# Optimization experiments

Measured on AMD Instinct MI355X. Metric: run time of the kernel, lower is better.

## Reference

```python
import jax, jax.numpy as jnp
import numpy as np

EPS = 1e-8
HALF_BIN = 0.1 / 2.0  # discretization_param / 2


def setup_inputs() -> dict:
    key = jax.random.key(0)
    k1, k2, k3, k4, k5, k6 = jax.random.split(key, 6)
    B, K = 4194304, 3
    predicted_purchase_prob = jax.random.uniform(k1, (B,), jnp.float32, 0.01, 0.99)
    mu = jax.random.normal(k2, (K, B), jnp.float32) * 5.0 + 10.0
    sigma = jax.random.uniform(k3, (K, B), jnp.float32, 0.1, 2.0)
    weight = jax.random.uniform(k4, (K, B), jnp.float32, 0.0, 1.0)
    paid = jax.random.uniform(k5, (B,)) > 0.5
    vals = jax.random.uniform(k6, (B,), jnp.float32, 0.1, 50.0)
    true_values = jnp.where(paid, vals, 0.0)
    return {
        "predicted_purchase_prob": predicted_purchase_prob,
        "mu": mu,
        "sigma": sigma,
        "weight": weight,
        "true_values": true_values,
    }


def reference(predicted_purchase_prob, mu, sigma, weight, true_values):
    p = predicted_purchase_prob  # [B]
    targets = (true_values > 0).astype(p.dtype)  # [B]
    # BCE with torch-style log clamping at -100
    log_p = jnp.clip(jnp.log(p + 0.0), -100.0)
    log_1mp = jnp.clip(jnp.log(1.0 - p), -100.0)
    purchase_loss = -jnp.mean(targets * log_p + (1.0 - targets) * log_1mp)

    # Mixture-of-logistics discretized likelihood, vectorized over [K, B]
    inv_s = 1.0 / (sigma + EPS)  # [K, B]
    tv = true_values[None, :]  # [1, B]
    cdf_upper = jax.nn.sigmoid((tv + HALF_BIN - mu) * inv_s)
    cdf_lower = jax.nn.sigmoid((tv - HALF_BIN - mu) * inv_s)
    prob_density = jnp.maximum(cdf_upper - cdf_lower, EPS)  # clamp(min=1e-8)
    likelihood = jnp.sum(weight * prob_density, axis=0)  # [B]
    log_likelihood = jnp.log(likelihood + EPS)  # [B]

    paid_mask = true_values > 0
    n_paid = jnp.sum(paid_mask.astype(p.dtype))
    ll_sum = jnp.sum(jnp.where(paid_mask, log_likelihood, 0.0))
    ltv_loss = -jnp.where(n_paid > 0, ll_sum / jnp.maximum(n_paid, 1.0), 0.0)

    return purchase_loss + ltv_loss
```

## Files before the change

### kernel.cpp

```cpp
#include <hip/hip_runtime.h>
#include <math.h>

#define EPS 1e-8f
#define HALF_BIN 0.05f

typedef float v4f __attribute__((ext_vector_type(4)));

#define GLOAD4(dst, addr) \
    asm("global_load_dwordx4 %0, %1, off" : "=v"(dst) : "v"(addr))

__device__ __forceinline__ float sigmoid_diff(float xu, float xl) {
    float eu = __expf(fminf(-xu, 87.0f));
    float el = __expf(fminf(-xl, 87.0f));
    return __fdividef(el - eu, (1.0f + eu) * (1.0f + el));
}

__device__ __forceinline__ void accum4(
    const v4f& pf, const v4f& tf,
    const v4f& m0, const v4f& s0, const v4f& w0,
    const v4f& m1, const v4f& s1, const v4f& w1,
    const v4f& m2, const v4f& s2, const v4f& w2,
    float& bce, float& ll, float& npaid)
{
    float lik[4] = {0.0f, 0.0f, 0.0f, 0.0f};
    const v4f* mm[3] = {&m0, &m1, &m2};
    const v4f* ss[3] = {&s0, &s1, &s2};
    const v4f* ww[3] = {&w0, &w1, &w2};
    #pragma unroll
    for (int k = 0; k < 3; ++k) {
        const v4f m = *mm[k], s = *ss[k], w = *ww[k];
        #pragma unroll
        for (int j = 0; j < 4; ++j) {
            float inv_s = __fdividef(1.0f, s[j] + EPS);
            float xu = (tf[j] + HALF_BIN - m[j]) * inv_s;
            float xl = (tf[j] - HALF_BIN - m[j]) * inv_s;
            float pd = fmaxf(sigmoid_diff(xu, xl), EPS);
            lik[j] = fmaf(w[j], pd, lik[j]);
        }
    }
    #pragma unroll
    for (int j = 0; j < 4; ++j) {
        bool paid = tf[j] > 0.0f;
        float val = paid ? pf[j] : (1.0f - pf[j]);
        bce -= fmaxf(__logf(val), -100.0f);
        float lg = __logf(lik[j] + EPS);
        ll    += paid ? lg : 0.0f;
        npaid += paid ? 1.0f : 0.0f;
    }
}

__global__ __launch_bounds__(256, 4) void zimol_main_k3(
    const float* __restrict__ p,
    const float* __restrict__ mu,
    const float* __restrict__ sigma,
    const float* __restrict__ weight,
    const float* __restrict__ tv,
    float* __restrict__ part_bce,
    float* __restrict__ part_ll,
    float* __restrict__ part_n,
    int B)
{
    const int tid    = blockIdx.x * blockDim.x + threadIdx.x;
    const int stride = gridDim.x * blockDim.x;
    const size_t B4  = (size_t)(B >> 2);

    const v4f* __restrict__ p4  = (const v4f*)p;
    const v4f* __restrict__ tv4 = (const v4f*)tv;
    const v4f* __restrict__ mu4 = (const v4f*)mu;
    const v4f* __restrict__ sg4 = (const v4f*)sigma;
    const v4f* __restrict__ wt4 = (const v4f*)weight;

    float bce = 0.0f, ll = 0.0f, npaid = 0.0f;

    for (size_t i = (size_t)tid; i < B4; i += (size_t)stride) {
        v4f bp, bt, bm0, bs0, bw0, bm1, bs1, bw1, bm2, bs2, bw2;
        GLOAD4(bp,  p4  + i);
        GLOAD4(bt,  tv4 + i);
        GLOAD4(bm0, mu4 + i);
        GLOAD4(bs0, sg4 + i);
        GLOAD4(bw0, wt4 + i);
        GLOAD4(bm1, mu4 + B4 + i);
        GLOAD4(bs1, sg4 + B4 + i);
        GLOAD4(bw1, wt4 + B4 + i);
        GLOAD4(bm2, mu4 + 2 * B4 + i);
        GLOAD4(bs2, sg4 + 2 * B4 + i);
        GLOAD4(bw2, wt4 + 2 * B4 + i);
        asm volatile("s_waitcnt vmcnt(0)"
                     : "+v"(bp), "+v"(bt),
                       "+v"(bm0), "+v"(bs0), "+v"(bw0),
                       "+v"(bm1), "+v"(bs1), "+v"(bw1),
                       "+v"(bm2), "+v"(bs2), "+v"(bw2));
        accum4(bp, bt, bm0, bs0, bw0, bm1, bs1, bw1, bm2, bs2, bw2,
               bce, ll, npaid);
    }

    #pragma unroll
    for (int off = 32; off > 0; off >>= 1) {
        bce   += __shfl_down(bce,   off, 64);
        ll    += __shfl_down(ll,    off, 64);
        npaid += __shfl_down(npaid, off, 64);
    }
    __shared__ float sdata[3][4];
    const int wave = threadIdx.x >> 6;
    const int lane = threadIdx.x & 63;
    if (lane == 0) {
        sdata[0][wave] = bce; sdata[1][wave] = ll; sdata[2][wave] = npaid;
    }
    __syncthreads();
    if (threadIdx.x == 0) {
        float b = 0.0f, l = 0.0f, n = 0.0f;
        #pragma unroll
        for (int w = 0; w < 4; ++w) {
            b += sdata[0][w]; l += sdata[1][w]; n += sdata[2][w];
        }
        part_bce[blockIdx.x] = b;
        part_ll [blockIdx.x] = l;
        part_n  [blockIdx.x] = n;
    }
}

template <int K>
__global__ __launch_bounds__(256) void zimol_main_gen(
    const float* __restrict__ p,
    const float* __restrict__ mu,
    const float* __restrict__ sigma,
    const float* __restrict__ weight,
    const float* __restrict__ tv,
    float* __restrict__ part_bce,
    float* __restrict__ part_ll,
    float* __restrict__ part_n,
    int B)
{
    const int tid    = blockIdx.x * blockDim.x + threadIdx.x;
    const int stride = gridDim.x * blockDim.x;

    float bce = 0.0f, ll = 0.0f, npaid = 0.0f;

    for (int i = tid; i < B; i += stride) {
        float t = tv[i];
        float lik = 0.0f;
        #pragma unroll
        for (int k = 0; k < K; ++k) {
            size_t off = (size_t)k * (size_t)B + (size_t)i;
            float inv_s = __fdividef(1.0f, sigma[off] + EPS);
            float xu = (t + HALF_BIN - mu[off]) * inv_s;
            float xl = (t - HALF_BIN - mu[off]) * inv_s;
            float pd = fmaxf(sigmoid_diff(xu, xl), EPS);
            lik = fmaf(weight[off], pd, lik);
        }
        bool paid = t > 0.0f;
        float val = paid ? p[i] : (1.0f - p[i]);
        bce -= fmaxf(__logf(val), -100.0f);
        float lg = __logf(lik + EPS);
        ll    += paid ? lg : 0.0f;
        npaid += paid ? 1.0f : 0.0f;
    }

    #pragma unroll
    for (int off = 32; off > 0; off >>= 1) {
        bce   += __shfl_down(bce,   off, 64);
        ll    += __shfl_down(ll,    off, 64);
        npaid += __shfl_down(npaid, off, 64);
    }
    __shared__ float sdata[3][4];
    const int wave = threadIdx.x >> 6;
    const int lane = threadIdx.x & 63;
    if (lane == 0) {
        sdata[0][wave] = bce; sdata[1][wave] = ll; sdata[2][wave] = npaid;
    }
    __syncthreads();
    if (threadIdx.x == 0) {
        float b = 0.0f, l = 0.0f, n = 0.0f;
        #pragma unroll
        for (int w = 0; w < 4; ++w) {
            b += sdata[0][w]; l += sdata[1][w]; n += sdata[2][w];
        }
        part_bce[blockIdx.x] = b;
        part_ll [blockIdx.x] = l;
        part_n  [blockIdx.x] = n;
    }
}

__global__ __launch_bounds__(256) void zimol_reduce(
    const float* __restrict__ part_bce,
    const float* __restrict__ part_ll,
    const float* __restrict__ part_n,
    float* __restrict__ out, int nblocks, int B)
{
    double b = 0.0, l = 0.0, n = 0.0;
    for (int i = threadIdx.x; i < nblocks; i += 256) {
        b += (double)part_bce[i];
        l += (double)part_ll[i];
        n += (double)part_n[i];
    }
    #pragma unroll
    for (int off = 32; off > 0; off >>= 1) {
        b += __shfl_down(b, off, 64);
        l += __shfl_down(l, off, 64);
        n += __shfl_down(n, off, 64);
    }
    __shared__ double sdata[3][4];
    const int wave = threadIdx.x >> 6;
    const int lane = threadIdx.x & 63;
    if (lane == 0) {
        sdata[0][wave] = b; sdata[1][wave] = l; sdata[2][wave] = n;
    }
    __syncthreads();
    if (threadIdx.x == 0) {
        double tb = 0.0, tl = 0.0, tn = 0.0;
        #pragma unroll
        for (int w = 0; w < 4; ++w) {
            tb += sdata[0][w]; tl += sdata[1][w]; tn += sdata[2][w];
        }
        double purchase = tb / (double)B;
        double ltv = (tn > 0.0) ? -(tl / fmax(tn, 1.0)) : 0.0;
        out[0] = (float)(purchase + ltv);
    }
}

extern "C" void kernel_launch(void* const* d_in, const int* in_sizes, int n_in,
                              void* d_out, int out_size, void* d_ws, size_t ws_size,
                              hipStream_t stream) {
    const float* p      = (const float*)d_in[0];
    const float* mu     = (const float*)d_in[1];
    const float* sigma  = (const float*)d_in[2];
    const float* weight = (const float*)d_in[3];
    const float* tv     = (const float*)d_in[4];
    float* out = (float*)d_out;

    const int B = in_sizes[0];
    const int K = in_sizes[1] / B;

    const int threads = 256;
    int blocks;

    float* part_bce = (float*)d_ws;

    if (K == 3 && (B & 3) == 0) {
        int work = B >> 2;
        blocks = (work + threads - 1) / threads;
        if (blocks > 2048) blocks = 2048;
        if (blocks < 1) blocks = 1;
        float* part_ll = part_bce + blocks;
        float* part_n  = part_ll  + blocks;
        zimol_main_k3<<<blocks, threads, 0, stream>>>(
            p, mu, sigma, weight, tv, part_bce, part_ll, part_n, B);
        zimol_reduce<<<1, threads, 0, stream>>>(part_bce, part_ll, part_n, out, blocks, B);
    } else {
        blocks = (B + threads - 1) / threads;
        if (blocks > 2048) blocks = 2048;
        if (blocks < 1) blocks = 1;
        float* part_ll = part_bce + blocks;
        float* part_n  = part_ll  + blocks;
        if (K == 1) {
            zimol_main_gen<1><<<blocks, threads, 0, stream>>>(
                p, mu, sigma, weight, tv, part_bce, part_ll, part_n, B);
        } else if (K == 2) {
            zimol_main_gen<2><<<blocks, threads, 0, stream>>>(
                p, mu, sigma, weight, tv, part_bce, part_ll, part_n, B);
        } else if (K == 3) {
            zimol_main_gen<3><<<blocks, threads, 0, stream>>>(
                p, mu, sigma, weight, tv, part_bce, part_ll, part_n, B);
        } else {
            zimol_main_gen<4><<<blocks, threads, 0, stream>>>(
                p, mu, sigma, weight, tv, part_bce, part_ll, part_n, B);
        }
        zimol_reduce<<<1, threads, 0, stream>>>(part_bce, part_ll, part_n, out, blocks, B);
    }
}
```

Measured before the change: 198.3 us.

## Double-buffer tiles in LDS via global_load_lds with wave-split async loads

Replaces direct per-thread dwordx4 register loads with asynchronous global-to-LDS loads (global_load_lds) into a double-buffered 512-element tile, split across the four waves. The next tile is prefetched while the current one is computed, using vmcnt waits and barriers for ordering. The grid is fixed at 768 blocks. This is meant to overlap memory latency with the transcendental-heavy compute, at the cost of two barriers per tile and a larger LDS footprint, which may lower occupancy.

```diff
diff --git a/kernel.cpp b/kernel.cpp
--- a/kernel.cpp
+++ b/kernel.cpp
@@ -4,10 +4,11 @@
 #define EPS 1e-8f
 #define HALF_BIN 0.05f
 
-typedef float v4f __attribute__((ext_vector_type(4)));
-
-#define GLOAD4(dst, addr) \
-    asm("global_load_dwordx4 %0, %1, off" : "=v"(dst) : "v"(addr))
+#define TILE 512
+#define BUF_FLOATS (11 * TILE)
+#define SMEM_FLOATS (2 * BUF_FLOATS)
+
+typedef float v2f __attribute__((ext_vector_type(2)));
 
 __device__ __forceinline__ float sigmoid_diff(float xu, float xl) {
     float eu = __expf(fminf(-xu, 87.0f));
@@ -15,41 +16,51 @@
     return __fdividef(el - eu, (1.0f + eu) * (1.0f + el));
 }
 
-__device__ __forceinline__ void accum4(
-    const v4f& pf, const v4f& tf,
-    const v4f& m0, const v4f& s0, const v4f& w0,
-    const v4f& m1, const v4f& s1, const v4f& w1,
-    const v4f& m2, const v4f& s2, const v4f& w2,
-    float& bce, float& ll, float& npaid)
+__device__ __forceinline__ void ld_unit(const float* gsrc, float* ldst_uniform) {
+    __builtin_amdgcn_global_load_lds(
+        (const __attribute__((address_space(1))) void*)gsrc,
+        (__attribute__((address_space(3))) void*)ldst_uniform,
+        16, 0, 0);
+}
+
+__device__ __forceinline__ void issue_tile(
+    const float* p, const float* tv,
+    const float* mu0, const float* sg0, const float* wt0,
+    const float* mu1, const float* sg1, const float* wt1,
+    const float* mu2, const float* sg2, const float* wt2,
+    float* lb, int tstart, int wave, int lane)
 {
-    float lik[4] = {0.0f, 0.0f, 0.0f, 0.0f};
-    const v4f* mm[3] = {&m0, &m1, &m2};
-    const v4f* ss[3] = {&s0, &s1, &s2};
-    const v4f* ww[3] = {&w0, &w1, &w2};
-    #pragma unroll
-    for (int k = 0; k < 3; ++k) {
-        const v4f m = *mm[k], s = *ss[k], w = *ww[k];
-        #pragma unroll
-        for (int j = 0; j < 4; ++j) {
-            float inv_s = __fdividef(1.0f, s[j] + EPS);
-            float xu = (tf[j] + HALF_BIN - m[j]) * inv_s;
-            float xl = (tf[j] - HALF_BIN - m[j]) * inv_s;
-            float pd = fmaxf(sigmoid_diff(xu, xl), EPS);
-            lik[j] = fmaf(w[j], pd, lik[j]);
-        }
-    }
-    #pragma unroll
-    for (int j = 0; j < 4; ++j) {
-        bool paid = tf[j] > 0.0f;
-        float val = paid ? pf[j] : (1.0f - pf[j]);
-        bce -= fmaxf(__logf(val), -100.0f);
-        float lg = __logf(lik[j] + EPS);
-        ll    += paid ? lg : 0.0f;
-        npaid += paid ? 1.0f : 0.0f;
-    }
-}
-
-__global__ __launch_bounds__(256, 4) void zimol_main_k3(
+    const int l4 = lane * 4;
+    if (wave == 0) {
+        ld_unit(p   + tstart       + l4, lb + 0);
+        ld_unit(p   + tstart + 256 + l4, lb + 256);
+        ld_unit(tv  + tstart       + l4, lb + 512);
+        ld_unit(tv  + tstart + 256 + l4, lb + 768);
+        ld_unit(mu0 + tstart       + l4, lb + 1024);
+        ld_unit(mu0 + tstart + 256 + l4, lb + 1280);
+    } else if (wave == 1) {
+        ld_unit(sg0 + tstart       + l4, lb + 1536);
+        ld_unit(sg0 + tstart + 256 + l4, lb + 1792);
+        ld_unit(wt0 + tstart       + l4, lb + 2048);
+        ld_unit(wt0 + tstart + 256 + l4, lb + 2304);
+        ld_unit(mu1 + tstart       + l4, lb + 2560);
+        ld_unit(mu1 + tstart + 256 + l4, lb + 2816);
+    } else if (wave == 2) {
+        ld_unit(sg1 + tstart       + l4, lb + 3072);
+        ld_unit(sg1 + tstart + 256 + l4, lb + 3328);
+        ld_unit(wt1 + tstart       + l4, lb + 3584);
+        ld_unit(wt1 + tstart + 256 + l4, lb + 3840);
+        ld_unit(mu2 + tstart       + l4, lb + 4096);
+    } else {
+        ld_unit(mu2 + tstart + 256 + l4, lb + 4352);
+        ld_unit(sg2 + tstart       + l4, lb + 4608);
+        ld_unit(sg2 + tstart + 256 + l4, lb + 4864);
+        ld_unit(wt2 + tstart       + l4, lb + 5120);
+        ld_unit(wt2 + tstart + 256 + l4, lb + 5376);
+    }
+}
+
+__global__ __launch_bounds__(256) void zimol_main_k3(
     const float* __restrict__ p,
     const float* __restrict__ mu,
     const float* __restrict__ sigma,
@@ -60,38 +71,84 @@
     float* __restrict__ part_n,
     int B)
 {
-    const int tid    = blockIdx.x * blockDim.x + threadIdx.x;
-    const int stride = gridDim.x * blockDim.x;
-    const size_t B4  = (size_t)(B >> 2);
-
-    const v4f* __restrict__ p4  = (const v4f*)p;
-    const v4f* __restrict__ tv4 = (const v4f*)tv;
-    const v4f* __restrict__ mu4 = (const v4f*)mu;
-    const v4f* __restrict__ sg4 = (const v4f*)sigma;
-    const v4f* __restrict__ wt4 = (const v4f*)weight;
+    __shared__ float smem[SMEM_FLOATS];
+
+    const int wave = threadIdx.x >> 6;
+    const int lane = threadIdx.x & 63;
+    const int nt   = B / TILE;
+    const int G    = gridDim.x;
+
+    const float* mu0 = mu;
+    const float* mu1 = mu + (size_t)B;
+    const float* mu2 = mu + 2 * (size_t)B;
+    const float* sg0 = sigma;
+    const float* sg1 = sigma + (size_t)B;
+    const float* sg2 = sigma + 2 * (size_t)B;
+    const float* wt0 = weight;
+    const float* wt1 = weight + (size_t)B;
+    const float* wt2 = weight + 2 * (size_t)B;
 
     float bce = 0.0f, ll = 0.0f, npaid = 0.0f;
 
-    for (size_t i = (size_t)tid; i < B4; i += (size_t)stride) {
-        v4f bp, bt, bm0, bs0, bw0, bm1, bs1, bw1, bm2, bs2, bw2;
-        GLOAD4(bp,  p4  + i);
-        GLOAD4(bt,  tv4 + i);
-        GLOAD4(bm0, mu4 + i);
-        GLOAD4(bs0, sg4 + i);
-        GLOAD4(bw0, wt4 + i);
-        GLOAD4(bm1, mu4 + B4 + i);
-        GLOAD4(bs1, sg4 + B4 + i);
-        GLOAD4(bw1, wt4 + B4 + i);
-        GLOAD4(bm2, mu4 + 2 * B4 + i);
-        GLOAD4(bs2, sg4 + 2 * B4 + i);
-        GLOAD4(bw2, wt4 + 2 * B4 + i);
-        asm volatile("s_waitcnt vmcnt(0)"
-                     : "+v"(bp), "+v"(bt),
-                       "+v"(bm0), "+v"(bs0), "+v"(bw0),
-                       "+v"(bm1), "+v"(bs1), "+v"(bw1),
-                       "+v"(bm2), "+v"(bs2), "+v"(bw2));
-        accum4(bp, bt, bm0, bs0, bw0, bm1, bs1, bw1, bm2, bs2, bw2,
-               bce, ll, npaid);
+    int t   = blockIdx.x;
+    int buf = 0;
+    if (t < nt)
+        issue_tile(p, tv, mu0, sg0, wt0, mu1, sg1, wt1, mu2, sg2, wt2,
+                   smem, t * TILE, wave, lane);
+
+    for (; t < nt; t += G) {
+        const int tn = t + G;
+        if (tn < nt) {
+            issue_tile(p, tv, mu0, sg0, wt0, mu1, sg1, wt1, mu2, sg2, wt2,
+                       smem + (buf ^ 1) * BUF_FLOATS, tn * TILE, wave, lane);
+            if (wave < 2) asm volatile("s_waitcnt vmcnt(6)" ::: "memory");
+            else          asm volatile("s_waitcnt vmcnt(5)" ::: "memory");
+        } else {
+            asm volatile("s_waitcnt vmcnt(0)" ::: "memory");
+        }
+        asm volatile("s_barrier" ::: "memory");
+
+        const float* lb = smem + buf * BUF_FLOATS;
+        const int e = 2 * threadIdx.x;
+
+        v2f P = *(const v2f*)(lb + 0   + e);
+        v2f T = *(const v2f*)(lb + 512 + e);
+        v2f M[3], S[3], W[3];
+        M[0] = *(const v2f*)(lb + 1024 + e);
+        S[0] = *(const v2f*)(lb + 1536 + e);
+        W[0] = *(const v2f*)(lb + 2048 + e);
+        M[1] = *(const v2f*)(lb + 2560 + e);
+        S[1] = *(const v2f*)(lb + 3072 + e);
+        W[1] = *(const v2f*)(lb + 3584 + e);
+        M[2] = *(const v2f*)(lb + 4096 + e);
+        S[2] = *(const v2f*)(lb + 4608 + e);
+        W[2] = *(const v2f*)(lb + 5120 + e);
+
+        float lik[2] = {0.0f, 0.0f};
+        #pragma unroll
+        for (int k = 0; k < 3; ++k) {
+            #pragma unroll
+            for (int j = 0; j < 2; ++j) {
+                float inv_s = __fdividef(1.0f, S[k][j] + EPS);
+                float xu = (T[j] + HALF_BIN - M[k][j]) * inv_s;
+                float xl = (T[j] - HALF_BIN - M[k][j]) * inv_s;
+                float pd = fmaxf(sigmoid_diff(xu, xl), EPS);
+                lik[j] = fmaf(W[k][j], pd, lik[j]);
+            }
+        }
+        #pragma unroll
+        for (int j = 0; j < 2; ++j) {
+            bool paid = T[j] > 0.0f;
+            float val = paid ? P[j] : (1.0f - P[j]);
+            bce -= fmaxf(__logf(val), -100.0f);
+            float lg = __logf(lik[j] + EPS);
+            ll    += paid ? lg : 0.0f;
+            npaid += paid ? 1.0f : 0.0f;
+        }
+
+        asm volatile("s_waitcnt lgkmcnt(0)" ::: "memory");
+        asm volatile("s_barrier" ::: "memory");
+        buf ^= 1;
     }
 
     #pragma unroll
@@ -101,8 +158,6 @@
         npaid += __shfl_down(npaid, off, 64);
     }
     __shared__ float sdata[3][4];
-    const int wave = threadIdx.x >> 6;
-    const int lane = threadIdx.x & 63;
     if (lane == 0) {
         sdata[0][wave] = bce; sdata[1][wave] = ll; sdata[2][wave] = npaid;
     }
@@ -232,22 +287,19 @@
     const int K = in_sizes[1] / B;
 
     const int threads = 256;
-    int blocks;
-
     float* part_bce = (float*)d_ws;
 
-    if (K == 3 && (B & 3) == 0) {
-        int work = B >> 2;
-        blocks = (work + threads - 1) / threads;
-        if (blocks > 2048) blocks = 2048;
-        if (blocks < 1) blocks = 1;
+    if (K == 3 && (B % TILE) == 0) {
+        int nt = B / TILE;
+        int blocks = 768;
+        if (blocks > nt) blocks = nt;
         float* part_ll = part_bce + blocks;
         float* part_n  = part_ll  + blocks;
         zimol_main_k3<<<blocks, threads, 0, stream>>>(
             p, mu, sigma, weight, tv, part_bce, part_ll, part_n, B);
         zimol_reduce<<<1, threads, 0, stream>>>(part_bce, part_ll, part_n, out, blocks, B);
     } else {
-        blocks = (B + threads - 1) / threads;
+        int blocks = (B + threads - 1) / threads;
         if (blocks > 2048) blocks = 2048;
         if (blocks < 1) blocks = 1;
         float* part_ll = part_bce + blocks;
```

Measured after the change: 199.3 us. Within noise of the previous version (+0.5%).
